# Kernel tuning notes

Hardware: AMD Instinct MI355X
Metric: run time of the kernel (lower is better)

Reference implementation:

```python
import jax, jax.numpy as jnp
import numpy as np

D_H = 128
N_RBF = 16
R_MIN = 0.0
R_MAX = float(np.sqrt(2.0))


def _rbf(r):
    # Gaussian RBF expansion: centers linspace(R_MIN, R_MAX, N_RBF),
    # width = center spacing, exp(-(r-mu)^2 / (2*width^2))
    centers = jnp.linspace(R_MIN, R_MAX, N_RBF, dtype=r.dtype)
    width = (R_MAX - R_MIN) / (N_RBF - 1)
    gamma = 1.0 / (2.0 * width * width)
    return jnp.exp(-gamma * (r[:, None] - centers[None, :]) ** 2)


def setup_inputs() -> dict:
    key = jax.random.key(0)
    ks = jax.random.split(key, 16)
    N, E = 50000, 800000
    h = jax.random.normal(ks[0], (N, D_H), dtype=jnp.float32)
    x = jax.random.uniform(ks[1], (N, 2), dtype=jnp.float32)
    edge_index = jax.random.randint(ks[2], (2, E), 0, N, dtype=jnp.int64)
    edge_weight = jax.random.uniform(ks[3], (E,), dtype=jnp.float32)

    def lin(k, fan_in, fan_out):
        s = 1.0 / np.sqrt(fan_in)
        kw, kb = jax.random.split(k)
        W = jax.random.uniform(kw, (fan_in, fan_out), minval=-s, maxval=s, dtype=jnp.float32)
        b = jax.random.uniform(kb, (fan_out,), minval=-s, maxval=s, dtype=jnp.float32)
        return W, b

    Wm1, bm1 = lin(ks[4], 2 * D_H + N_RBF, D_H)
    Wm2, bm2 = lin(ks[5], D_H, D_H)
    Wh1, bh1 = lin(ks[6], 2 * D_H, D_H)
    Wh2, bh2 = lin(ks[7], D_H, D_H)
    ln_g = jnp.ones((D_H,), dtype=jnp.float32)
    ln_b = jnp.zeros((D_H,), dtype=jnp.float32)
    return {"h": h, "x": x, "edge_index": edge_index, "edge_weight": edge_weight,
            "Wm1": Wm1, "bm1": bm1, "Wm2": Wm2, "bm2": bm2,
            "Wh1": Wh1, "bh1": bh1, "Wh2": Wh2, "bh2": bh2,
            "ln_g": ln_g, "ln_b": ln_b}


def reference(h, x, edge_index, edge_weight, Wm1, bm1, Wm2, bm2, Wh1, bh1, Wh2, bh2, ln_g, ln_b):
    N = h.shape[0]
    src = edge_index[0]
    dst = edge_index[1]
    # per-edge geometry
    dx = x[src, :2] - x[dst, :2]                      # [E,2]
    r = jnp.sqrt(jnp.sum(dx * dx, axis=-1) + 1e-8)    # [E]
    rbf = _rbf(r)                                     # [E,n_rbf]
    # message MLP: Linear -> SiLU -> Linear
    m_in = jnp.concatenate([h[src], h[dst], rbf], axis=-1)  # [E, 2*d_h+n_rbf]
    m = jax.nn.silu(m_in @ Wm1 + bm1) @ Wm2 + bm2            # [E, d_h]
    m = m * edge_weight[:, None]
    # scatter-sum aggregate into destination nodes
    agg = jax.ops.segment_sum(m, dst, num_segments=N)        # [N, d_h]
    # node update MLP
    u_in = jnp.concatenate([h, agg], axis=-1)                # [N, 2*d_h]
    h_up = jax.nn.silu(u_in @ Wh1 + bh1) @ Wh2 + bh2         # [N, d_h]
    # residual + LayerNorm
    z = h + h_up
    mu = jnp.mean(z, axis=-1, keepdims=True)
    var = jnp.var(z, axis=-1, keepdims=True)
    return (z - mu) / jnp.sqrt(var + 1e-5) * ln_g + ln_b
```

## Files before the change

### kernel.cpp

```cpp
#include <hip/hip_runtime.h>
#include <hip/hip_bf16.h>
#include <math.h>

#define DH 128
#define NRBF 16
#define EB 256
#define NTAB 1025
#define SEGCAP 32

typedef unsigned short ushort_t;
typedef __attribute__((ext_vector_type(8))) short short8;
typedef __attribute__((ext_vector_type(4))) float floatx4;

__device__ __forceinline__ float silu_f(float v) {
    return v / (1.f + __expf(-v));
}
__device__ __forceinline__ unsigned pk_bf16(float lo, float hi) {
    __hip_bfloat162 h = __float22bfloat162_rn(make_float2(lo, hi));
    union { __hip_bfloat162 h2; unsigned u; } cv;
    cv.h2 = h;
    return cv.u;
}
__device__ __forceinline__ ushort_t f2bf1(float f) {
    unsigned u = __float_as_uint(f);
    u += 0x7FFFu + ((u >> 16) & 1u);
    return (ushort_t)(u >> 16);
}
__device__ __forceinline__ float bflo(unsigned u) { return __uint_as_float(u << 16); }
__device__ __forceinline__ float bfhi(unsigned u) { return __uint_as_float(u & 0xffff0000u); }
__device__ __forceinline__ float bf2f(ushort_t u) { return __uint_as_float(((unsigned)u) << 16); }

__device__ __forceinline__ int detect64(const int* __restrict__ ei) {
    int z = 0;
#pragma unroll
    for (int i = 0; i < 8; ++i) z |= ei[2 * i + 1];
    return (z == 0) ? 1 : 0;
}
__device__ __forceinline__ int load_dst(const int* ei, int is64, int e, int E) {
    return is64 ? ei[2 * E + 2 * e] : ei[E + e];
}
__device__ __forceinline__ int load_src(const int* ei, int is64, int e, int E) {
    return is64 ? ei[2 * e] : ei[e];
}

__global__ __launch_bounds__(256) void k_hist_prep(
    const int* __restrict__ ei, int* __restrict__ counts, int E,
    const float* __restrict__ Wm1, const float* __restrict__ Wm2,
    const float* __restrict__ Wh1, const float* __restrict__ Wh2,
    ushort_t* __restrict__ Tbf, ushort_t* __restrict__ W2f,
    ushort_t* __restrict__ W1mf, ushort_t* __restrict__ W1hf,
    ushort_t* __restrict__ W2hf, int nb_hist)
{
    const int b = blockIdx.x, tid = threadIdx.x;
    if (b < nb_hist) {
        const int e = b * 256 + tid;
        if (e < E) {
            const int is64 = detect64(ei);
            atomicAdd(&counts[load_dst(ei, is64, e, E)], 1);
        }
        return;
    }
    int b2 = b - nb_hist;
    if (b2 < 257) {
        const int i = b2 * 4 + (tid >> 6);
        if (i < NTAB) {
            const float WIDTH = 0.09428090415820634f;
            const float GAMMA = 56.25f;
            const float DELTA = 1.4142135623730951f / 1024.0f;
            const float r = (float)i * DELTA;
            const int c0 = (tid & 63) * 2;
            float a0 = 0.f, a1 = 0.f;
#pragma unroll
            for (int q = 0; q < NRBF; ++q) {
                const float dr = r - (float)q * WIDTH;
                const float w = __expf(-GAMMA * dr * dr);
                a0 = fmaf(w, Wm1[(256 + q) * DH + c0], a0);
                a1 = fmaf(w, Wm1[(256 + q) * DH + c0 + 1], a1);
            }
            *(unsigned*)(Tbf + (size_t)i * DH + c0) = pk_bf16(a0, a1);
        }
        return;
    }
    b2 -= 257;
    if (b2 < 8) {
        const int u = b2 * 256 + tid;
        const int col = u & 127, kclg = u >> 7;
        const int lg = kclg & 3, kc = kclg >> 2;
        unsigned o[4];
#pragma unroll
        for (int j = 0; j < 2; ++j) {
            o[j]     = pk_bf16(Wm2[(kc * 32 + 4 * lg + 2 * j) * DH + col],
                               Wm2[(kc * 32 + 4 * lg + 2 * j + 1) * DH + col]);
            o[2 + j] = pk_bf16(Wm2[(kc * 32 + 16 + 4 * lg + 2 * j) * DH + col],
                               Wm2[(kc * 32 + 16 + 4 * lg + 2 * j + 1) * DH + col]);
        }
        *(uint4*)(W2f + 8 * u) = make_uint4(o[0], o[1], o[2], o[3]);
        return;
    }
    b2 -= 8;
    if (b2 < 16) {
        const int u = b2 * 256 + tid;
        const int c = u & 255, kclg = u >> 8;
        const int lg = kclg & 3, kc = kclg >> 2;
        const int base = (c < 128) ? 0 : 128;
        const int cc = c & 127;
        unsigned o[4];
#pragma unroll
        for (int j = 0; j < 2; ++j) {
            o[j]     = pk_bf16(Wm1[(base + kc * 32 + 4 * lg + 2 * j) * DH + cc],
                               Wm1[(base + kc * 32 + 4 * lg + 2 * j + 1) * DH + cc]);
            o[2 + j] = pk_bf16(Wm1[(base + kc * 32 + 16 + 4 * lg + 2 * j) * DH + cc],
                               Wm1[(base + kc * 32 + 16 + 4 * lg + 2 * j + 1) * DH + cc]);
        }
        *(uint4*)(W1mf + 8 * u) = make_uint4(o[0], o[1], o[2], o[3]);
        return;
    }
    b2 -= 16;
    if (b2 < 16) {
        const int u = b2 * 256 + tid;
        const int col = u & 127, kclg = u >> 7;
        const int lg = kclg & 3, kc = kclg >> 2;
        unsigned o[4];
#pragma unroll
        for (int j = 0; j < 2; ++j) {
            o[j]     = pk_bf16(Wh1[(kc * 32 + 4 * lg + 2 * j) * DH + col],
                               Wh1[(kc * 32 + 4 * lg + 2 * j + 1) * DH + col]);
            o[2 + j] = pk_bf16(Wh1[(kc * 32 + 16 + 4 * lg + 2 * j) * DH + col],
                               Wh1[(kc * 32 + 16 + 4 * lg + 2 * j + 1) * DH + col]);
        }
        *(uint4*)(W1hf + 8 * u) = make_uint4(o[0], o[1], o[2], o[3]);
        return;
    }
    b2 -= 16;
    {
        const int u = b2 * 256 + tid;
        const int col = u & 127, kclg = u >> 7;
        const int lg = kclg & 3, kc = kclg >> 2;
        unsigned o[4];
#pragma unroll
        for (int j = 0; j < 2; ++j) {
            o[j]     = pk_bf16(Wh2[(kc * 32 + 4 * lg + 2 * j) * DH + col],
                               Wh2[(kc * 32 + 4 * lg + 2 * j + 1) * DH + col]);
            o[2 + j] = pk_bf16(Wh2[(kc * 32 + 16 + 4 * lg + 2 * j) * DH + col],
                               Wh2[(kc * 32 + 16 + 4 * lg + 2 * j + 1) * DH + col]);
        }
        *(uint4*)(W2hf + 8 * u) = make_uint4(o[0], o[1], o[2], o[3]);
    }
}

__global__ __launch_bounds__(1024) void k_scan(const int* __restrict__ counts,
                                               int* __restrict__ cursor, int N) {
    __shared__ int wsum[16];
    __shared__ int sCarry;
    const int tid = threadIdx.x, lane = tid & 63, wid = tid >> 6;
    if (tid == 0) sCarry = 0;
    __syncthreads();
    for (int c0 = 0; c0 < N; c0 += 4096) {
        const int idx = c0 + tid * 4;
        int4 v = make_int4(0, 0, 0, 0);
        if (idx < N) v = *(const int4*)(counts + idx);
        const int t01 = v.x + v.y;
        const int t012 = t01 + v.z;
        const int tot = t012 + v.w;
        int incl = tot;
#pragma unroll
        for (int d = 1; d < 64; d <<= 1) {
            int t = __shfl_up(incl, d, 64);
            if (lane >= d) incl += t;
        }
        if (lane == 63) wsum[wid] = incl;
        __syncthreads();
        if (wid == 0) {
            int s = (lane < 16) ? wsum[lane] : 0;
#pragma unroll
            for (int d = 1; d < 16; d <<= 1) {
                int t = __shfl_up(s, d, 64);
                if (lane >= d) s += t;
            }
            if (lane < 16) wsum[lane] = s;
        }
        __syncthreads();
        const int ex = sCarry + (wid > 0 ? wsum[wid - 1] : 0) + incl - tot;
        if (idx + 3 < N) {
            *(int4*)(cursor + idx) = make_int4(ex, ex + v.x, ex + t01, ex + t012);
        } else if (idx < N) {
            cursor[idx] = ex;
            if (idx + 1 < N) cursor[idx + 1] = ex + v.x;
            if (idx + 2 < N) cursor[idx + 2] = ex + t01;
        }
        __syncthreads();
        if (tid == 0) sCarry += wsum[15];
        __syncthreads();
    }
}

__global__ __launch_bounds__(256) void k_scatter_pre(
    const int* __restrict__ ei, const float* __restrict__ ew, const float* __restrict__ x,
    int* __restrict__ cursor, uint4* __restrict__ epk,
    int E, int pack,
    const float* __restrict__ h, const float* __restrict__ bm1,
    const ushort_t* __restrict__ W1mf,
    ushort_t* __restrict__ Abf, ushort_t* __restrict__ Bbf, int N, int nb_scat)
{
    const int tid = threadIdx.x;

    if ((int)blockIdx.x < nb_scat) {
        const int e = blockIdx.x * 256 + tid;
        if (e < E) {
            const int is64 = detect64(ei);
            const int s = load_src(ei, is64, e, E);
            const int d = load_dst(ei, is64, e, E);
            const int pos = atomicAdd(&cursor[d], 1);
            unsigned x0 = (unsigned)s;
            if (pack) {
                const float2 xs = *(const float2*)(x + 2 * s);
                const float2 xd = *(const float2*)(x + 2 * d);
                const float dxv = xs.x - xd.x, dyv = xs.y - xd.y;
                const float r = sqrtf(dxv * dxv + dyv * dyv + 1e-8f);
                int ti = (int)(r * 724.0773439350246f + 0.5f);
                ti = min(ti, NTAB - 1);
                x0 |= ((unsigned)ti << 16);
            }
            epk[pos] = make_uint4(x0, __float_as_uint(ew[e]), (unsigned)d, 0u);
        }
        return;
    }

    __shared__ __align__(16) ushort_t sIn[64 * DH];
    const int nblk = ((int)blockIdx.x - nb_scat) * 64;

    {
        const int row = tid >> 2, q = tid & 3;
        const int gn = nblk + row;
        const float4* ps = (const float4*)(h + (size_t)gn * DH + 32 * q);
        uint4* rowp = (uint4*)(sIn + row * DH);
        const int swz = row & 7;
#pragma unroll
        for (int i = 0; i < 4; ++i) {
            uint4 o = make_uint4(0, 0, 0, 0);
            if (gn < N) {
                const float4 g0 = ps[2 * i], g1 = ps[2 * i + 1];
                o.x = pk_bf16(g0.x, g0.y); o.y = pk_bf16(g0.z, g0.w);
                o.z = pk_bf16(g1.x, g1.y); o.w = pk_bf16(g1.z, g1.w);
            }
            rowp[(4 * q + i) ^ swz] = o;
        }
    }
    __syncthreads();

    const int lane = tid & 63, wv = tid >> 6;
    const int lr = lane & 15, lg = lane >> 4;
    const int m0l = wv * 16;

    union FragU { unsigned u[4]; short8 s8; };
    floatx4 acc[16];
#pragma unroll
    for (int ni = 0; ni < 16; ++ni) acc[ni] = (floatx4){0.f, 0.f, 0.f, 0.f};

#pragma unroll
    for (int kc = 0; kc < 4; ++kc) {
        const int b1 = 64 * kc + 8 * lg;
        const int b2 = b1 + 32;
        const int row = m0l + lr;
        const char* rbase = (const char*)(sIn + row * DH);
        const int swz = (row & 7) << 4;
        FragU af;
        const uint2 lo = *(const uint2*)(rbase + ((b1 & ~15) ^ swz) + (b1 & 15));
        const uint2 hi = *(const uint2*)(rbase + ((b2 & ~15) ^ swz) + (b2 & 15));
        af.u[0] = lo.x; af.u[1] = lo.y; af.u[2] = hi.x; af.u[3] = hi.y;
        const ushort_t* wbase = W1mf + ((size_t)(kc * 4 + lg) * 256 + lr) * 8;
        __builtin_amdgcn_s_setprio(1);
#pragma unroll
        for (int ni = 0; ni < 16; ++ni) {
            const short8 bf = *(const short8*)(wbase + ni * 128);
            acc[ni] = __builtin_amdgcn_mfma_f32_16x16x32_bf16(af.s8, bf, acc[ni], 0, 0, 0);
        }
        __builtin_amdgcn_s_setprio(0);
    }

    float bm1v[8];
#pragma unroll
    for (int ni = 0; ni < 8; ++ni) bm1v[ni] = bm1[ni * 16 + lr];
#pragma unroll
    for (int r = 0; r < 4; ++r) {
        const int gn = nblk + m0l + 4 * lg + r;
        if (gn < N) {
#pragma unroll
            for (int ni = 0; ni < 8; ++ni)
                Abf[(size_t)gn * DH + ni * 16 + lr] = f2bf1(acc[ni][r] + bm1v[ni]);
#pragma unroll
            for (int ni = 8; ni < 16; ++ni)
                Bbf[(size_t)gn * DH + (ni - 8) * 16 + lr] = f2bf1(acc[ni][r]);
        }
    }
}

__global__ __launch_bounds__(256) void k_build(
    const float* __restrict__ x, const uint4* __restrict__ epk,
    const ushort_t* __restrict__ Abf, const ushort_t* __restrict__ Bbf,
    const ushort_t* __restrict__ Tbf, ushort_t* __restrict__ Hbf,
    int pack, int E)
{
    const int gid = blockIdx.x * 256 + threadIdx.x;
    const int e = gid >> 2, q = gid & 3;
    if (e >= E) return;

    const uint4 v = epk[e];
    const int d = (int)v.z;
    int s, ti;
    if (pack) { s = (int)(v.x & 0xFFFFu); ti = (int)(v.x >> 16); }
    else {
        s = (int)v.x;
        const float2 xs = *(const float2*)(x + 2 * s);
        const float2 xd = *(const float2*)(x + 2 * d);
        const float dxv = xs.x - xd.x, dyv = xs.y - xd.y;
        const float r = sqrtf(dxv * dxv + dyv * dyv + 1e-8f);
        ti = min((int)(r * 724.0773439350246f + 0.5f), NTAB - 1);
    }

    const uint4* pA = (const uint4*)(Abf + (size_t)s * DH + 32 * q);
    const uint4* pB = (const uint4*)(Bbf + (size_t)d * DH + 32 * q);
    const uint4* pT = (const uint4*)(Tbf + (size_t)ti * DH + 32 * q);
    uint4 av[4], bv[4], tv[4];
#pragma unroll
    for (int i = 0; i < 4; ++i) { av[i] = pA[i]; bv[i] = pB[i]; tv[i] = pT[i]; }

    uint4* rowp = (uint4*)(Hbf + (size_t)e * DH);
    const int swz = e & 7;
#pragma unroll
    for (int i = 0; i < 4; ++i) {
        const uint4 a = av[i]; const uint4 b = bv[i]; const uint4 t = tv[i];
        const float v0 = bflo(a.x) + bflo(b.x) + bflo(t.x);
        const float v1 = bfhi(a.x) + bfhi(b.x) + bfhi(t.x);
        const float v2 = bflo(a.y) + bflo(b.y) + bflo(t.y);
        const float v3 = bfhi(a.y) + bfhi(b.y) + bfhi(t.y);
        const float v4 = bflo(a.z) + bflo(b.z) + bflo(t.z);
        const float v5 = bfhi(a.z) + bfhi(b.z) + bfhi(t.z);
        const float v6 = bflo(a.w) + bflo(b.w) + bflo(t.w);
        const float v7 = bfhi(a.w) + bfhi(b.w) + bfhi(t.w);
        uint4 pk;
        pk.x = pk_bf16(silu_f(v0), silu_f(v1));
        pk.y = pk_bf16(silu_f(v2), silu_f(v3));
        pk.z = pk_bf16(silu_f(v4), silu_f(v5));
        pk.w = pk_bf16(silu_f(v6), silu_f(v7));
        rowp[(4 * q + i) ^ swz] = pk;
    }
}

__global__ __launch_bounds__(256, 4) void k_gemm(
    const uint4* __restrict__ epk, const ushort_t* __restrict__ Hbf,
    const ushort_t* __restrict__ W2f, const float* __restrict__ bm2,
    float* __restrict__ agg, int N, int E)
{
    __shared__ __align__(16) ushort_t sHid[4][16 * DH];
    __shared__ __align__(16) float ldsAgg[SEGCAP][DH];
    __shared__ int   sDst[EB];
    __shared__ int   sLid[EB];
    __shared__ float sEw[EB];
    __shared__ int   sSegStart[SEGCAP];
    __shared__ int   sNseg;
    __shared__ int   sWtot[4];

    const int tid  = threadIdx.x;
    const int lane = tid & 63;
    const int wv   = tid >> 6;
    const int lr   = lane & 15;
    const int lg   = lane >> 4;
    const int e4   = lane >> 2;
    const int q    = lane & 3;
    const int wbase = wv * 64;

    const int nwg = gridDim.x;
    const int xcd = blockIdx.x & 7;
    const int cidx = blockIdx.x >> 3;
    const int qch = nwg >> 3, rch = nwg & 7;
    const int bid = (xcd < rch) ? (xcd * (qch + 1) + cidx)
                                : (rch * (qch + 1) + (xcd - rch) * qch + cidx);
    const int e0 = bid * EB;

    {
        const float4 z = make_float4(0.f, 0.f, 0.f, 0.f);
        float4* za = (float4*)&ldsAgg[0][0];
#pragma unroll
        for (int i = 0; i < 4; ++i) za[tid + 256 * i] = z;
    }

    {
        const int slot = e0 + tid;
        int d;
        float w = 0.f;
        if (slot < E) {
            const uint4 v = epk[slot];
            w = __uint_as_float(v.y);
            d = (int)v.z;
        } else {
            d = (int)epk[E - 1].z;
        }
        sDst[tid] = d; sEw[tid] = w;
    }
    __syncthreads();

    {
        const int bflag = (tid > 0) && (sDst[tid] != sDst[tid - 1]);
        int incl = bflag;
#pragma unroll
        for (int dd = 1; dd < 64; dd <<= 1) {
            int t = __shfl_up(incl, dd, 64);
            if (lane >= dd) incl += t;
        }
        if (lane == 63) sWtot[wv] = incl;
        __syncthreads();
        int off = 0;
#pragma unroll
        for (int wq = 0; wq < 3; ++wq)
            if (wq < wv) off += sWtot[wq];
        incl += off;
        sLid[tid] = incl;
        if ((bflag || tid == 0) && incl < SEGCAP) sSegStart[incl] = tid;
        if (tid == EB - 1) sNseg = incl + 1;
    }
    __syncthreads();

    float bc8[8];
#pragma unroll
    for (int ni = 0; ni < 8; ++ni) bc8[ni] = bm2[ni * 16 + lr];

    union FragU { unsigned u[4]; short8 s8; };
    ushort_t* slice = &sHid[wv][0];
    floatx4 acc[8];

#pragma unroll
    for (int st = 0; st < 4; ++st) {
        const int sb = wbase + st * 16;
        const int le = sb + e4;

        {
            const uint4* gsrc = (const uint4*)(Hbf + (size_t)(e0 + le) * DH);
            uint4* rowp = (uint4*)(slice + e4 * DH);
            const int swz = e4 & 7;
#pragma unroll
            for (int i = 0; i < 4; ++i) {
                const int c = (4 * q + i) ^ swz;
                rowp[c] = gsrc[c];
            }
        }

#pragma unroll
        for (int ni = 0; ni < 8; ++ni) acc[ni] = (floatx4){0.f, 0.f, 0.f, 0.f};
#pragma unroll
        for (int kc = 0; kc < 4; ++kc) {
            const int bo1 = 64 * kc + 8 * lg;
            const int bo2 = bo1 + 32;
            const char* rbase = (const char*)(slice + lr * DH);
            const int swzf = (lr & 7) << 4;
            FragU af;
            const uint2 lo = *(const uint2*)(rbase + ((bo1 & ~15) ^ swzf) + (bo1 & 15));
            const uint2 hi = *(const uint2*)(rbase + ((bo2 & ~15) ^ swzf) + (bo2 & 15));
            af.u[0] = lo.x; af.u[1] = lo.y; af.u[2] = hi.x; af.u[3] = hi.y;
            const ushort_t* wb2 = W2f + ((size_t)(kc * 4 + lg) * 128 + lr) * 8;
            __builtin_amdgcn_s_setprio(1);
#pragma unroll
            for (int ni = 0; ni < 8; ++ni) {
                const short8 bf = *(const short8*)(wb2 + ni * 128);
                acc[ni] = __builtin_amdgcn_mfma_f32_16x16x32_bf16(af.s8, bf, acc[ni], 0, 0, 0);
            }
            __builtin_amdgcn_s_setprio(0);
        }

        {
            const int sbg = sb + 4 * lg;
            int lid4[4]; float ew4[4];
#pragma unroll
            for (int r = 0; r < 4; ++r) { lid4[r] = sLid[sbg + r]; ew4[r] = sEw[sbg + r]; }
#pragma unroll
            for (int ni = 0; ni < 8; ++ni) {
                const int col = ni * 16 + lr;
                const float bc = bc8[ni];
                int cur = lid4[0], curSlot = sbg;
                float avv = (acc[ni][0] + bc) * ew4[0];
#pragma unroll
                for (int r = 1; r < 4; ++r) {
                    const int l2 = lid4[r];
                    const float v = (acc[ni][r] + bc) * ew4[r];
                    if (l2 == cur) avv += v;
                    else {
                        if (cur < SEGCAP) atomicAdd(&ldsAgg[cur][col], avv);
                        else atomicAdd(agg + (size_t)sDst[curSlot] * DH + col, avv);
                        cur = l2; curSlot = sbg + r; avv = v;
                    }
                }
                if (cur < SEGCAP) atomicAdd(&ldsAgg[cur][col], avv);
                else atomicAdd(agg + (size_t)sDst[curSlot] * DH + col, avv);
            }
        }
    }

    __syncthreads();

    const int ns = sNseg;
    const int gmax = (ns < SEGCAP) ? ns : SEGCAP;
    for (int idx = tid; idx < (gmax << 7); idx += 256) {
        const int g = idx >> 7, col = idx & 127;
        const float v = ldsAgg[g][col];
        const int dst = sDst[sSegStart[g]];
        float* p = agg + (size_t)dst * DH + col;
        if (g > 0 && g < ns - 1) *p = v;
        else atomicAdd(p, v);
    }
}

__global__ __launch_bounds__(256, 2) void k_edge_mono(
    const float* __restrict__ x, const int* __restrict__ ei, const float* __restrict__ ew,
    const uint4* __restrict__ epk,
    const ushort_t* __restrict__ W2f, const float* __restrict__ bm2,
    const ushort_t* __restrict__ Abf, const ushort_t* __restrict__ Bbf,
    const ushort_t* __restrict__ Tbf, float* __restrict__ agg,
    int sorted, int pack, int N, int E)
{
    __shared__ __align__(16) ushort_t sHid[4][16 * DH];
    __shared__ __align__(16) float ldsAgg[SEGCAP][DH];
    __shared__ int   sSrc[EB];
    __shared__ int   sDst[EB];
    __shared__ int   sLid[EB];
    __shared__ int   sTi[EB];
    __shared__ float sEw[EB];
    __shared__ int   sSegStart[SEGCAP];
    __shared__ int   sNseg;
    __shared__ int   sWtot[4];

    const int tid  = threadIdx.x;
    const int lane = tid & 63;
    const int wv   = tid >> 6;
    const int lr   = lane & 15;
    const int lg   = lane >> 4;
    const int e4   = lane >> 2;
    const int q    = lane & 3;
    const int wbase = wv * 64;

    const int nwg = gridDim.x;
    const int xcd = blockIdx.x & 7;
    const int cidx = blockIdx.x >> 3;
    const int qch = nwg >> 3, rch = nwg & 7;
    const int bid = (xcd < rch) ? (xcd * (qch + 1) + cidx)
                                : (rch * (qch + 1) + (xcd - rch) * qch + cidx);
    const int e0 = bid * EB;

    {
        const float4 z = make_float4(0.f, 0.f, 0.f, 0.f);
        float4* za = (float4*)&ldsAgg[0][0];
#pragma unroll
        for (int i = 0; i < 4; ++i) za[tid + 256 * i] = z;
    }

    {
        const int slot = e0 + tid;
        int s = 0, d = 0, ti = 0;
        float w = 0.f;
        if (slot < E) {
            if (sorted) {
                const uint4 v = epk[slot];
                w = __uint_as_float(v.y);
                d = (int)v.z;
                if (pack) { s = (int)(v.x & 0xFFFFu); ti = (int)(v.x >> 16); }
                else {
                    s = (int)v.x;
                    const float2 xs = *(const float2*)(x + 2 * s);
                    const float2 xd = *(const float2*)(x + 2 * d);
                    const float dxv = xs.x - xd.x, dyv = xs.y - xd.y;
                    const float r = sqrtf(dxv * dxv + dyv * dyv + 1e-8f);
                    ti = min((int)(r * 724.0773439350246f + 0.5f), NTAB - 1);
                }
            } else {
                const int is64 = detect64(ei);
                s = load_src(ei, is64, slot, E);
                d = load_dst(ei, is64, slot, E);
                w = ew[slot];
                const float2 xs = *(const float2*)(x + 2 * s);
                const float2 xd = *(const float2*)(x + 2 * d);
                const float dxv = xs.x - xd.x, dyv = xs.y - xd.y;
                const float r = sqrtf(dxv * dxv + dyv * dyv + 1e-8f);
                ti = min((int)(r * 724.0773439350246f + 0.5f), NTAB - 1);
            }
        } else {
            d = sorted ? (int)epk[E - 1].z : load_dst(ei, detect64(ei), E - 1, E);
        }
        sSrc[tid] = s; sDst[tid] = d; sEw[tid] = w; sTi[tid] = ti;
    }
    __syncthreads();

    {
        const int bflag = (tid > 0) && (sDst[tid] != sDst[tid - 1]);
        int incl = bflag;
#pragma unroll
        for (int dd = 1; dd < 64; dd <<= 1) {
            int t = __shfl_up(incl, dd, 64);
            if (lane >= dd) incl += t;
        }
        if (lane == 63) sWtot[wv] = incl;
        __syncthreads();
        int off = 0;
#pragma unroll
        for (int wq = 0; wq < 3; ++wq)
            if (wq < wv) off += sWtot[wq];
        incl += off;
        sLid[tid] = incl;
        if ((bflag || tid == 0) && incl < SEGCAP) sSegStart[incl] = tid;
        if (tid == EB - 1) sNseg = incl + 1;
    }
    __syncthreads();

    float bc8[8];
#pragma unroll
    for (int ni = 0; ni < 8; ++ni) bc8[ni] = bm2[ni * 16 + lr];

    union FragU { unsigned u[4]; short8 s8; };
    ushort_t* slice = &sHid[wv][0];
    floatx4 acc[8];

#pragma unroll
    for (int st = 0; st < 4; ++st) {
        const int sb = wbase + st * 16;
        const int le = sb + e4;
        const int s  = sSrc[le];
        const int d  = sDst[le];
        const int ti = sTi[le];
        const uint4* pA = (const uint4*)(Abf + (size_t)s * DH + 32 * q);
        const uint4* pB = (const uint4*)(Bbf + (size_t)d * DH + 32 * q);
        const uint4* pT = (const uint4*)(Tbf + (size_t)ti * DH + 32 * q);
        uint4 av[4], bv[4], tv[4];
#pragma unroll
        for (int i = 0; i < 4; ++i) { av[i] = pA[i]; bv[i] = pB[i]; tv[i] = pT[i]; }

        {
            uint4* rowp = (uint4*)(slice + e4 * DH);
            const int swzw = e4 & 7;
#pragma unroll
            for (int i = 0; i < 4; ++i) {
                const uint4 a = av[i]; const uint4 b = bv[i]; const uint4 t = tv[i];
                const float v0 = bflo(a.x) + bflo(b.x) + bflo(t.x);
                const float v1 = bfhi(a.x) + bfhi(b.x) + bfhi(t.x);
                const float v2 = bflo(a.y) + bflo(b.y) + bflo(t.y);
                const float v3 = bfhi(a.y) + bfhi(b.y) + bfhi(t.y);
                const float v4 = bflo(a.z) + bflo(b.z) + bflo(t.z);
                const float v5 = bfhi(a.z) + bfhi(b.z) + bfhi(t.z);
                const float v6 = bflo(a.w) + bflo(b.w) + bflo(t.w);
                const float v7 = bfhi(a.w) + bfhi(b.w) + bfhi(t.w);
                uint4 pk;
                pk.x = pk_bf16(silu_f(v0), silu_f(v1));
                pk.y = pk_bf16(silu_f(v2), silu_f(v3));
                pk.z = pk_bf16(silu_f(v4), silu_f(v5));
                pk.w = pk_bf16(silu_f(v6), silu_f(v7));
                rowp[(4 * q + i) ^ swzw] = pk;
            }
        }

#pragma unroll
        for (int ni = 0; ni < 8; ++ni) acc[ni] = (floatx4){0.f, 0.f, 0.f, 0.f};
#pragma unroll
        for (int kc = 0; kc < 4; ++kc) {
            const int bo1 = 64 * kc + 8 * lg;
            const int bo2 = bo1 + 32;
            const char* rbase = (const char*)(slice + lr * DH);
            const int swzf = (lr & 7) << 4;
            FragU af;
            const uint2 lo = *(const uint2*)(rbase + ((bo1 & ~15) ^ swzf) + (bo1 & 15));
            const uint2 hi = *(const uint2*)(rbase + ((bo2 & ~15) ^ swzf) + (bo2 & 15));
            af.u[0] = lo.x; af.u[1] = lo.y; af.u[2] = hi.x; af.u[3] = hi.y;
            const ushort_t* wb2 = W2f + ((size_t)(kc * 4 + lg) * 128 + lr) * 8;
            __builtin_amdgcn_s_setprio(1);
#pragma unroll
            for (int ni = 0; ni < 8; ++ni) {
                const short8 bf = *(const short8*)(wb2 + ni * 128);
                acc[ni] = __builtin_amdgcn_mfma_f32_16x16x32_bf16(af.s8, bf, acc[ni], 0, 0, 0);
            }
            __builtin_amdgcn_s_setprio(0);
        }

        {
            const int sbg = sb + 4 * lg;
            int lid4[4]; float ew4[4];
#pragma unroll
            for (int r = 0; r < 4; ++r) { lid4[r] = sLid[sbg + r]; ew4[r] = sEw[sbg + r]; }
#pragma unroll
            for (int ni = 0; ni < 8; ++ni) {
                const int col = ni * 16 + lr;
                const float bc = bc8[ni];
                int cur = lid4[0], curSlot = sbg;
                float avv = (acc[ni][0] + bc) * ew4[0];
#pragma unroll
                for (int r = 1; r < 4; ++r) {
                    const int l2 = lid4[r];
                    const float v = (acc[ni][r] + bc) * ew4[r];
                    if (l2 == cur) avv += v;
                    else {
                        if (cur < SEGCAP) atomicAdd(&ldsAgg[cur][col], avv);
                        else atomicAdd(agg + (size_t)sDst[curSlot] * DH + col, avv);
                        cur = l2; curSlot = sbg + r; avv = v;
                    }
                }
                if (cur < SEGCAP) atomicAdd(&ldsAgg[cur][col], avv);
                else atomicAdd(agg + (size_t)sDst[curSlot] * DH + col, avv);
            }
        }
    }

    __syncthreads();

    const int ns = sNseg;
    const int gmax = (ns < SEGCAP) ? ns : SEGCAP;
    for (int idx = tid; idx < (gmax << 7); idx += 256) {
        const int g = idx >> 7, col = idx & 127;
        const float v = ldsAgg[g][col];
        const int dst = sDst[sSegStart[g]];
        float* p = agg + (size_t)dst * DH + col;
        if (sorted && g > 0 && g < ns - 1) *p = v;
        else atomicAdd(p, v);
    }
}

__global__ __launch_bounds__(256) void k_node(
    const float* __restrict__ h, const float* __restrict__ agg,
    const ushort_t* __restrict__ W1hf, const float* __restrict__ bh1,
    const ushort_t* __restrict__ W2hf, const float* __restrict__ bh2,
    const float* __restrict__ ln_g, const float* __restrict__ ln_b,
    float* __restrict__ out, int N)
{
    __shared__ __align__(16) ushort_t sIn[64 * 256];
    __shared__ __align__(16) ushort_t sHid[64 * DH];
    const int tid = threadIdx.x;
    const int nblk = blockIdx.x * 64;

    {
        const int row = tid >> 2, q = tid & 3;
        const int gn = nblk + row;
        const float4* ps = (q < 2) ? (const float4*)(h + (size_t)gn * DH + 64 * q)
                                   : (const float4*)(agg + (size_t)gn * DH + 64 * (q - 2));
        uint4* rowp = (uint4*)(sIn + row * 256);
        const int swz = row & 7;
#pragma unroll
        for (int i = 0; i < 8; ++i) {
            uint4 o = make_uint4(0, 0, 0, 0);
            if (gn < N) {
                const float4 g0 = ps[2 * i], g1 = ps[2 * i + 1];
                o.x = pk_bf16(g0.x, g0.y); o.y = pk_bf16(g0.z, g0.w);
                o.z = pk_bf16(g1.x, g1.y); o.w = pk_bf16(g1.z, g1.w);
            }
            rowp[(8 * q + i) ^ swz] = o;
        }
    }
    __syncthreads();

    const int lane = tid & 63, wv = tid >> 6;
    const int lr = lane & 15, lg = lane >> 4;
    const int m0l = wv * 16;

    union FragU { unsigned u[4]; short8 s8; };

    floatx4 acc[8];
#pragma unroll
    for (int ni = 0; ni < 8; ++ni) acc[ni] = (floatx4){0.f, 0.f, 0.f, 0.f};

#pragma unroll
    for (int kc = 0; kc < 8; ++kc) {
        const int b1 = 64 * kc + 8 * lg;
        const int b2 = b1 + 32;
        const int row = m0l + lr;
        const char* rbase = (const char*)(sIn + row * 256);
        const int swz = (row & 7) << 4;
        FragU af;
        const uint2 lo = *(const uint2*)(rbase + ((b1 & ~15) ^ swz) + (b1 & 15));
        const uint2 hi = *(const uint2*)(rbase + ((b2 & ~15) ^ swz) + (b2 & 15));
        af.u[0] = lo.x; af.u[1] = lo.y; af.u[2] = hi.x; af.u[3] = hi.y;
        const ushort_t* wbase = W1hf + ((size_t)(kc * 4 + lg) * 128 + lr) * 8;
        __builtin_amdgcn_s_setprio(1);
#pragma unroll
        for (int ni = 0; ni < 8; ++ni) {
            const short8 bf = *(const short8*)(wbase + ni * 128);
            acc[ni] = __builtin_amdgcn_mfma_f32_16x16x32_bf16(af.s8, bf, acc[ni], 0, 0, 0);
        }
        __builtin_amdgcn_s_setprio(0);
    }

    {
        float bh1v[8];
#pragma unroll
        for (int ni = 0; ni < 8; ++ni) bh1v[ni] = bh1[ni * 16 + lr];
#pragma unroll
        for (int r = 0; r < 4; ++r) {
            const int row = m0l + 4 * lg + r;
            const int swz = row & 7;
            ushort_t* rp = sHid + row * DH;
#pragma unroll
            for (int ni = 0; ni < 8; ++ni) {
                const int col = ni * 16 + lr;
                rp[(((col >> 3) ^ swz) << 3) + (col & 7)] =
                    f2bf1(silu_f(acc[ni][r] + bh1v[ni]));
            }
        }
    }

    floatx4 acc2[8];
#pragma unroll
    for (int ni = 0; ni < 8; ++ni) acc2[ni] = (floatx4){0.f, 0.f, 0.f, 0.f};

#pragma unroll
    for (int kc = 0; kc < 4; ++kc) {
        const int b1 = 64 * kc + 8 * lg;
        const int b2 = b1 + 32;
        const int row = m0l + lr;
        const char* rbase = (const char*)(sHid + row * DH);
        const int swz = (row & 7) << 4;
        FragU af;
        const uint2 lo = *(const uint2*)(rbase + ((b1 & ~15) ^ swz) + (b1 & 15));
        const uint2 hi = *(const uint2*)(rbase + ((b2 & ~15) ^ swz) + (b2 & 15));
        af.u[0] = lo.x; af.u[1] = lo.y; af.u[2] = hi.x; af.u[3] = hi.y;
        const ushort_t* wbase = W2hf + ((size_t)(kc * 4 + lg) * 128 + lr) * 8;
        __builtin_amdgcn_s_setprio(1);
#pragma unroll
        for (int ni = 0; ni < 8; ++ni) {
            const short8 bf = *(const short8*)(wbase + ni * 128);
            acc2[ni] = __builtin_amdgcn_mfma_f32_16x16x32_bf16(af.s8, bf, acc2[ni], 0, 0, 0);
        }
        __builtin_amdgcn_s_setprio(0);
    }

    float gv[8], bv[8], b2v[8];
#pragma unroll
    for (int ni = 0; ni < 8; ++ni) {
        const int col = ni * 16 + lr;
        gv[ni] = ln_g[col]; bv[ni] = ln_b[col]; b2v[ni] = bh2[col];
    }
#pragma unroll
    for (int r = 0; r < 4; ++r) {
        const int row = m0l + 4 * lg + r;
        const int gn = nblk + row;
        const int swz = row & 7;
        float z[8];
        float s1 = 0.f, s2 = 0.f;
#pragma unroll
        for (int ni = 0; ni < 8; ++ni) {
            const int col = ni * 16 + lr;
            const float hv = bf2f(sIn[row * 256 + (((col >> 3) ^ swz) << 3) + (col & 7)]);
            z[ni] = acc2[ni][r] + b2v[ni] + hv;
            s1 += z[ni]; s2 += z[ni] * z[ni];
        }
#pragma unroll
        for (int m = 1; m < 16; m <<= 1) {
            s1 += __shfl_xor(s1, m, 64);
            s2 += __shfl_xor(s2, m, 64);
        }
        const float mean = s1 * (1.f / 128.f);
        const float var = s2 * (1.f / 128.f) - mean * mean;
        const float rstd = rsqrtf(var + 1e-5f);
        if (gn < N) {
#pragma unroll
            for (int ni = 0; ni < 8; ++ni) {
                const int col = ni * 16 + lr;
                out[(size_t)gn * DH + col] = (z[ni] - mean) * rstd * gv[ni] + bv[ni];
            }
        }
    }
}

extern "C" void kernel_launch(void* const* d_in, const int* in_sizes, int n_in,
                              void* d_out, int out_size, void* d_ws, size_t ws_size,
                              hipStream_t stream)
{
    (void)n_in; (void)out_size;
    const float* h   = (const float*)d_in[0];
    const float* x   = (const float*)d_in[1];
    const int*   ei  = (const int*)d_in[2];
    const float* ew  = (const float*)d_in[3];
    const float* Wm1 = (const float*)d_in[4];
    const float* bm1 = (const float*)d_in[5];
    const float* Wm2 = (const float*)d_in[6];
    const float* bm2 = (const float*)d_in[7];
    const float* Wh1 = (const float*)d_in[8];
    const float* bh1 = (const float*)d_in[9];
    const float* Wh2 = (const float*)d_in[10];
    const float* bh2 = (const float*)d_in[11];
    const float* lng = (const float*)d_in[12];
    const float* lnb = (const float*)d_in[13];
    float* out = (float*)d_out;

    const int N = in_sizes[0] / DH;
    const int E = in_sizes[3];
    const int nbE = (E + EB - 1) / EB;

    float*    agg  = (float*)d_ws;
    int*   counts  = (int*)(agg + (size_t)N * DH);
    int*   cursor  = counts + N;
    ushort_t* Abf  = (ushort_t*)((((uintptr_t)(cursor + N)) + 15) & ~(uintptr_t)15);
    ushort_t* Bbf  = Abf + (size_t)N * DH;
    ushort_t* W2f  = Bbf + (size_t)N * DH;
    ushort_t* Tbf  = W2f + 16384;
    ushort_t* W1mf = Tbf + (size_t)NTAB * DH;
    ushort_t* W1hf = W1mf + 32768;
    ushort_t* W2hf = W1hf + 32768;
    uint4* epk     = (uint4*)((((uintptr_t)(W2hf + 16384)) + 15) & ~(uintptr_t)15);
    ushort_t* Hbf  = (ushort_t*)(epk + E);

    const size_t need_sort  = ((char*)(epk + E)) - ((char*)d_ws);
    const size_t need_split = need_sort + (size_t)nbE * EB * DH * sizeof(ushort_t);
    const int use_sort  = (ws_size >= need_sort) ? 1 : 0;
    const int use_split = use_sort && (ws_size >= need_split);
    const int pack = use_sort && (N <= 65535);

    const int nb_hist = use_sort ? (E + 255) / 256 : 0;
    const int nb_prep = 257 + 8 + 16 + 16 + 8;
    const int nb_scat = nb_hist;
    const int nb_pre  = (N + 63) / 64;

    hipMemsetAsync(agg, 0, (size_t)N * DH * sizeof(float) + (use_sort ? (size_t)N * 4 : 0), stream);
    k_hist_prep<<<nb_hist + nb_prep, 256, 0, stream>>>(ei, counts, E, Wm1, Wm2, Wh1, Wh2,
                                                       Tbf, W2f, W1mf, W1hf, W2hf, nb_hist);
    if (use_sort)
        k_scan<<<1, 1024, 0, stream>>>(counts, cursor, N);
    k_scatter_pre<<<nb_scat + nb_pre, 256, 0, stream>>>(ei, ew, x, cursor, epk, E, pack,
                                                        h, bm1, W1mf, Abf, Bbf, N, nb_scat);
    if (use_split) {
        k_build<<<(4 * E + 255) / 256, 256, 0, stream>>>(x, epk, Abf, Bbf, Tbf, Hbf, pack, E);
        k_gemm<<<nbE, 256, 0, stream>>>(epk, Hbf, W2f, bm2, agg, N, E);
    } else {
        k_edge_mono<<<nbE, 256, 0, stream>>>(x, ei, ew, epk, W2f, bm2, Abf, Bbf, Tbf, agg,
                                             use_sort, pack, N, E);
    }
    k_node<<<(N + 63) / 64, 256, 0, stream>>>(h, agg, W1hf, bh1, W2hf, bh2, lng, lnb, out, N);
}
```

Measured before the change: 385.0 us.

## Chunk edge build/GEMM to fit workspace and stage W2 in LDS

The split build+GEMM path now processes edges in chunks sized to the spare workspace, instead of needing a full E×128 bf16 hidden buffer. This lets the split path run when the workspace is too small, and keeps the hidden buffer small enough that it may stay in cache between build and GEMM. The GEMM kernel also copies the 32KB W2 matrix into shared memory per block and lowers the occupancy hint from 4 to 2. In exchange there are more kernel launches, per-block W2 copies, and possibly lower occupancy.

```diff
diff --git a/kernel.cpp b/kernel.cpp
--- a/kernel.cpp
+++ b/kernel.cpp
@@ -299,11 +299,12 @@
     const float* __restrict__ x, const uint4* __restrict__ epk,
     const ushort_t* __restrict__ Abf, const ushort_t* __restrict__ Bbf,
     const ushort_t* __restrict__ Tbf, ushort_t* __restrict__ Hbf,
-    int pack, int E)
+    int pack, int ce0, int cE, int E)
 {
     const int gid = blockIdx.x * 256 + threadIdx.x;
-    const int e = gid >> 2, q = gid & 3;
-    if (e >= E) return;
+    const int el = gid >> 2, q = gid & 3;
+    if (el >= cE) return;
+    const int e = ce0 + el;
 
     const uint4 v = epk[e];
     const int d = (int)v.z;
@@ -325,8 +326,8 @@
 #pragma unroll
     for (int i = 0; i < 4; ++i) { av[i] = pA[i]; bv[i] = pB[i]; tv[i] = pT[i]; }
 
-    uint4* rowp = (uint4*)(Hbf + (size_t)e * DH);
-    const int swz = e & 7;
+    uint4* rowp = (uint4*)(Hbf + (size_t)el * DH);
+    const int swz = el & 7;
 #pragma unroll
     for (int i = 0; i < 4; ++i) {
         const uint4 a = av[i]; const uint4 b = bv[i]; const uint4 t = tv[i];
@@ -347,12 +348,13 @@
     }
 }
 
-__global__ __launch_bounds__(256, 4) void k_gemm(
+__global__ __launch_bounds__(256, 2) void k_gemm(
     const uint4* __restrict__ epk, const ushort_t* __restrict__ Hbf,
     const ushort_t* __restrict__ W2f, const float* __restrict__ bm2,
-    float* __restrict__ agg, int N, int E)
+    float* __restrict__ agg, int chunk_base, int N, int E)
 {
     __shared__ __align__(16) ushort_t sHid[4][16 * DH];
+    __shared__ __align__(16) ushort_t sW2f[16384];
     __shared__ __align__(16) float ldsAgg[SEGCAP][DH];
     __shared__ int   sDst[EB];
     __shared__ int   sLid[EB];
@@ -376,8 +378,15 @@
     const int qch = nwg >> 3, rch = nwg & 7;
     const int bid = (xcd < rch) ? (xcd * (qch + 1) + cidx)
                                 : (rch * (qch + 1) + (xcd - rch) * qch + cidx);
-    const int e0 = bid * EB;
-
+    const int e0 = chunk_base + bid * EB;
+    const int hrow0 = bid * EB;
+
+    {
+        const uint4* s4 = (const uint4*)W2f;
+        uint4* d4 = (uint4*)sW2f;
+#pragma unroll
+        for (int i = 0; i < 8; ++i) d4[tid + 256 * i] = s4[tid + 256 * i];
+    }
     {
         const float4 z = make_float4(0.f, 0.f, 0.f, 0.f);
         float4* za = (float4*)&ldsAgg[0][0];
@@ -435,7 +444,7 @@
         const int le = sb + e4;
 
         {
-            const uint4* gsrc = (const uint4*)(Hbf + (size_t)(e0 + le) * DH);
+            const uint4* gsrc = (const uint4*)(Hbf + (size_t)(hrow0 + le) * DH);
             uint4* rowp = (uint4*)(slice + e4 * DH);
             const int swz = e4 & 7;
 #pragma unroll
@@ -457,7 +466,7 @@
             const uint2 lo = *(const uint2*)(rbase + ((bo1 & ~15) ^ swzf) + (bo1 & 15));
             const uint2 hi = *(const uint2*)(rbase + ((bo2 & ~15) ^ swzf) + (bo2 & 15));
             af.u[0] = lo.x; af.u[1] = lo.y; af.u[2] = hi.x; af.u[3] = hi.y;
-            const ushort_t* wb2 = W2f + ((size_t)(kc * 4 + lg) * 128 + lr) * 8;
+            const ushort_t* wb2 = sW2f + ((kc * 4 + lg) * 128 + lr) * 8;
             __builtin_amdgcn_s_setprio(1);
 #pragma unroll
             for (int ni = 0; ni < 8; ++ni) {
@@ -900,11 +909,15 @@
     uint4* epk     = (uint4*)((((uintptr_t)(W2hf + 16384)) + 15) & ~(uintptr_t)15);
     ushort_t* Hbf  = (ushort_t*)(epk + E);
 
-    const size_t need_sort  = ((char*)(epk + E)) - ((char*)d_ws);
-    const size_t need_split = need_sort + (size_t)nbE * EB * DH * sizeof(ushort_t);
-    const int use_sort  = (ws_size >= need_sort) ? 1 : 0;
-    const int use_split = use_sort && (ws_size >= need_split);
+    const size_t need_sort = ((char*)(epk + E)) - ((char*)d_ws);
+    const int use_sort = (ws_size >= need_sort) ? 1 : 0;
     const int pack = use_sort && (N <= 65535);
+
+    const size_t spare = use_sort ? (ws_size - need_sort) : 0;
+    size_t cblk = spare / ((size_t)EB * DH * sizeof(ushort_t));
+    if (cblk > (size_t)nbE) cblk = nbE;
+    const int chunk_blocks = (int)cblk;
+    const int use_split = use_sort && (chunk_blocks >= 64);
 
     const int nb_hist = use_sort ? (E + 255) / 256 : 0;
     const int nb_prep = 257 + 8 + 16 + 16 + 8;
@@ -919,8 +932,14 @@
     k_scatter_pre<<<nb_scat + nb_pre, 256, 0, stream>>>(ei, ew, x, cursor, epk, E, pack,
                                                         h, bm1, W1mf, Abf, Bbf, N, nb_scat);
     if (use_split) {
-        k_build<<<(4 * E + 255) / 256, 256, 0, stream>>>(x, epk, Abf, Bbf, Tbf, Hbf, pack, E);
-        k_gemm<<<nbE, 256, 0, stream>>>(epk, Hbf, W2f, bm2, agg, N, E);
+        for (int cb = 0; cb < nbE; cb += chunk_blocks) {
+            const int blocks = (nbE - cb < chunk_blocks) ? (nbE - cb) : chunk_blocks;
+            const int ce0 = cb * EB;
+            const int cE = (E - ce0 < blocks * EB) ? (E - ce0) : (blocks * EB);
+            k_build<<<(4 * cE + 255) / 256, 256, 0, stream>>>(x, epk, Abf, Bbf, Tbf, Hbf,
+                                                              pack, ce0, cE, E);
+            k_gemm<<<blocks, 256, 0, stream>>>(epk, Hbf, W2f, bm2, agg, ce0, N, E);
+        }
     } else {
         k_edge_mono<<<nbE, 256, 0, stream>>>(x, ei, ew, epk, W2f, bm2, Abf, Bbf, Tbf, agg,
                                              use_sort, pack, N, E);
```

Result: slower. 496.2 us (+28.9%).
